# Kernel tuning notes

Measured on AMD Instinct MI355X. Metric: run time of the kernel, lower is better.

## Reference

```python
import jax, jax.numpy as jnp
import numpy as np

N_NODES = 27
SRC = jnp.array([0,1,1,1,1,2,2,2,3,3,3,4,4,4,5,5,5,5,6,6,6,6,6,7,7,7,8,8,8,9,9,9,10,10,10,11,11,11,12,12,12,13,13,13,14,14,14,15,15,15,16,16,16,17,17,17,18,18,18,18,19,20,21,21,21,22,23,23,23,24,25,26], dtype=jnp.int32)
DST = jnp.array([1,0,2,4,6,1,3,7,2,4,24,1,3,5,4,6,17,19,1,5,7,8,10,2,6,23,6,9,16,8,10,13,6,9,11,10,12,23,11,13,21,9,12,14,13,15,20,14,16,18,8,15,17,5,16,18,15,17,25,26,5,14,12,22,23,21,7,11,21,3,18,18], dtype=jnp.int32)


def _conv2d(x, w, b):
    # x: [BN, Cin, H, W], w: [Cout, Cin, 3, 3] -> SAME padding conv
    y = jax.lax.conv_general_dilated(x, w, window_strides=(1, 1), padding='SAME',
                                     dimension_numbers=('NCHW', 'OIHW', 'NCHW'))
    return y + b[None, :, None, None]


def _block(h, w, b):
    # h: [B, N, Cin, H, W]; Conv2dMessage (conv -> scatter-add over edges) + LeakyReLU(0.2) + MaxPool2d(2)
    B, N, C, H, W = h.shape
    y = _conv2d(h.reshape(B * N, C, H, W), w, b).reshape(B, N, -1, H, W)
    # propagate with aggr='add': out[dst] += y[src]; isolated-in nodes become zero
    agg = jnp.zeros_like(y).at[:, DST].add(y[:, SRC])
    a = jax.nn.leaky_relu(agg, negative_slope=0.2)
    Co = a.shape[2]
    p = jax.lax.reduce_window(a.reshape(B * N, Co, H, W), -jnp.inf, jax.lax.max,
                              (1, 1, 2, 2), (1, 1, 2, 2), 'VALID')
    return p.reshape(B, N, Co, H // 2, W // 2)


def setup_inputs() -> dict:
    key = jax.random.key(0)
    ks = jax.random.split(key, 9)
    B, Cin, H, W = 32, 4, 64, 64
    x = jax.random.normal(ks[0], (B, Cin, H, W), dtype=jnp.float32)
    def kaiming(k, shape):
        fan_in = int(np.prod(shape[1:]))
        bound = float(np.sqrt(6.0 / fan_in))
        return jax.random.uniform(k, shape, jnp.float32, -bound, bound)
    w1 = kaiming(ks[1], (32, Cin, 3, 3)); b1 = jnp.zeros((32,), jnp.float32)
    w2 = kaiming(ks[2], (64, 32, 3, 3));  b2 = jnp.zeros((64,), jnp.float32)
    w3 = kaiming(ks[3], (128, 64, 3, 3)); b3 = jnp.zeros((128,), jnp.float32)
    wc = kaiming(ks[4], (1, 128));        bc = jnp.zeros((1,), jnp.float32)
    return {"x": x, "w1": w1, "b1": b1, "w2": w2, "b2": b2,
            "w3": w3, "b3": b3, "wc": wc, "bc": bc}


def reference(x, w1, b1, w2, b2, w3, b3, wc, bc):
    B = x.shape[0]
    # torch.tile(xi, (27,1,1,1)) vectorized over batch -> [B, 27, C, H, W]
    h = jnp.broadcast_to(x[:, None], (B, N_NODES) + x.shape[1:])
    h = _block(h, w1, b1)   # [B, 27, 32, 32, 32]
    h = _block(h, w2, b2)   # [B, 27, 64, 16, 16]
    h = _block(h, w3, b3)   # [B, 27, 128, 8, 8]
    feat = h.mean(axis=(3, 4))                 # AdaptiveAvgPool2d(1) + flatten -> [B, 27, 128]
    logits = jnp.einsum('bnc,oc->bno', feat, wc) + bc  # [B, 27, 1]
    return logits[:, 0, :]                     # classifier(xi)[0] per sample -> [B, 1]
```

## Files before the change

### kernel.cpp

```cpp
#include <hip/hip_runtime.h>


#define LRELU(v) fmaxf((v), 0.2f * (v))

#define P1H_ELEMS (32 * 32 * 34 * 36)
#define P2H_ELEMS (32 * 64 * 18 * 20)

__global__ __launch_bounds__(256, 4) void k1(const float* __restrict__ x,
                                             const float* __restrict__ w1,
                                             const float* __restrict__ b1,
                                             float* __restrict__ P1H,
                                             float* __restrict__ out) {
    __shared__ __align__(16) float obuf[1152];
    const int bx = blockIdx.x;
    const int b  = blockIdx.y;
    const int rb = bx & 3, cog = bx >> 2;
    const int t  = threadIdx.x;
    const int l  = t & 63, wv = t >> 6;
    const int r  = l >> 4, q = l & 15;
    const int row0 = 16 * rb + 4 * wv + r;

    if (bx == 0 && t == 0) out[b] = 0.f;

    for (int i = t; i < 288; i += 256)
        *(float4*)&obuf[4 * i] = make_float4(0.f, 0.f, 0.f, 0.f);
    __syncthreads();

    const bool cL = (q > 0), cR = (q < 15);
    const int colL = max(4 * q - 2, 0);
    const int colR = min(4 * q + 4, 62);

    float acc[4][4];
    #pragma unroll
    for (int g = 0; g < 4; ++g) {
        float bias = b1[cog * 4 + g];
        acc[g][0] = bias; acc[g][1] = bias; acc[g][2] = bias; acc[g][3] = bias;
    }

    #pragma unroll
    for (int c = 0; c < 4; ++c) {
        float win[3][6];
        #pragma unroll
        for (int d = 0; d < 3; ++d) {
            int gr = row0 - 1 + d;
            bool v = (unsigned)gr < 64u;
            int grc = min(max(gr, 0), 63);
            const float* row = x + ((b * 4 + c) * 64 + grc) * 64;
            float2 L  = *(const float2*)(row + colL);
            float4 M  = *(const float4*)(row + 4 * q);
            float2 R2 = *(const float2*)(row + colR);
            win[d][0] = (v && cL) ? L.y : 0.f;
            win[d][1] = v ? M.x : 0.f;
            win[d][2] = v ? M.y : 0.f;
            win[d][3] = v ? M.z : 0.f;
            win[d][4] = v ? M.w : 0.f;
            win[d][5] = (v && cR) ? R2.x : 0.f;
        }
        #pragma unroll
        for (int g = 0; g < 4; ++g) {
            const float* wp = &w1[((cog * 4 + g) * 4 + c) * 9];
            #pragma unroll
            for (int d = 0; d < 3; ++d)
                #pragma unroll
                for (int j = 0; j < 3; ++j) {
                    float w = wp[3 * d + j];
                    acc[g][0] += w * win[d][j];
                    acc[g][1] += w * win[d][j + 1];
                    acc[g][2] += w * win[d][j + 2];
                    acc[g][3] += w * win[d][j + 3];
                }
        }
    }

    const int prow_l = 2 * wv + (r >> 1);
    #pragma unroll
    for (int g = 0; g < 4; ++g) {
        float m0 = fmaxf(LRELU(acc[g][0]), LRELU(acc[g][1]));
        float m1 = fmaxf(LRELU(acc[g][2]), LRELU(acc[g][3]));
        float p0 = fmaxf(m0, __shfl_xor(m0, 16));
        float p1 = fmaxf(m1, __shfl_xor(m1, 16));
        if ((r & 1) == 0) {
            obuf[(g * 8 + prow_l) * 36 + 2 * q + 1] = 12.f * p0;
            obuf[(g * 8 + prow_l) * 36 + 2 * q + 2] = 12.f * p1;
        }
    }
    __syncthreads();

    for (int i = t; i < 288; i += 256) {
        int co_l = i / 72, rem = i % 72, pr = rem / 9, cw = rem % 9;
        *(float4*)&P1H[((b * 32 + cog * 4 + co_l) * 34 + 8 * rb + pr + 1) * 36 + 4 * cw] =
            *(const float4*)&obuf[4 * i];
    }
    if (rb == 0 || rb == 3) {
        int h = rb ? 33 : 0;
        for (int i = t; i < 36; i += 256) {
            int co_l = i / 9, cw = i % 9;
            *(float4*)&P1H[((b * 32 + cog * 4 + co_l) * 34 + h) * 36 + 4 * cw] =
                make_float4(0.f, 0.f, 0.f, 0.f);
        }
    }
}

__global__ __launch_bounds__(256, 2) void k2(const float* __restrict__ P1H,
                                             const float* __restrict__ w2,
                                             const float* __restrict__ b2,
                                             float* __restrict__ p2H) {
    __shared__ __align__(16) float wtile[6144];
    __shared__ __align__(16) float xin[2880];
    __shared__ __align__(16) float obuf[1280];
    const int bx = blockIdx.x;
    const int b  = blockIdx.y;
    const int cog = bx >> 2, rs = bx & 3;
    const int c0  = cog * 16;
    const int t  = threadIdx.x, l = t & 63;
    const int wvs = __builtin_amdgcn_readfirstlane(t >> 6);
    const int q  = l & 7, R = l >> 3;

    for (int i = t; i < 1152; i += 256) {
        float4 v = *(const float4*)&w2[cog * 4608 + 4 * i];
        int e = 4 * i;
        wtile[((e + 0) / 9) * 12 + (e + 0) % 9] = v.x;
        wtile[((e + 1) / 9) * 12 + (e + 1) % 9] = v.y;
        wtile[((e + 2) / 9) * 12 + (e + 2) % 9] = v.z;
        wtile[((e + 3) / 9) * 12 + (e + 3) % 9] = v.w;
    }
    for (int i = t; i < 320; i += 256)
        *(float4*)&obuf[4 * i] = make_float4(0.f, 0.f, 0.f, 0.f);

    float acc[4][4];
    #pragma unroll
    for (int g = 0; g < 4; ++g) {
        float bias = 4.f * b2[c0 + wvs * 4 + g];
        acc[g][0] = bias; acc[g][1] = bias; acc[g][2] = bias; acc[g][3] = bias;
    }

    for (int cc = 0; cc < 4; ++cc) {
        __syncthreads();
        for (int i = t; i < 720; i += 256) {
            int cin_l = i / 90, rem = i % 90;
            *(float4*)&xin[cin_l * 360 + 4 * rem] =
                *(const float4*)&P1H[((b * 32 + cc * 8 + cin_l) * 34 + rs * 8) * 36 + 4 * rem];
        }
        __syncthreads();
        #pragma unroll
        for (int cl = 0; cl < 8; ++cl) {
            float win[3][6];
            #pragma unroll
            for (int d = 0; d < 3; ++d) {
                const float* xr = &xin[cl * 360 + (R + d) * 36 + 4 * q];
                float4 M  = *(const float4*)xr;
                float2 Rt = *(const float2*)(xr + 4);
                win[d][0] = M.x; win[d][1] = M.y; win[d][2] = M.z;
                win[d][3] = M.w; win[d][4] = Rt.x; win[d][5] = Rt.y;
            }
            const int cin = cc * 8 + cl;
            #pragma unroll
            for (int g = 0; g < 4; ++g) {
                const float* wg = &wtile[((wvs * 4 + g) * 32 + cin) * 12];
                float4 wa = *(const float4*)wg;
                float4 wb = *(const float4*)(wg + 4);
                float  w8 = wg[8];
                float wt[9] = {wa.x, wa.y, wa.z, wa.w, wb.x, wb.y, wb.z, wb.w, w8};
                #pragma unroll
                for (int d = 0; d < 3; ++d)
                    #pragma unroll
                    for (int j = 0; j < 3; ++j) {
                        float w = wt[3 * d + j];
                        acc[g][0] += w * win[d][j];
                        acc[g][1] += w * win[d][j + 1];
                        acc[g][2] += w * win[d][j + 2];
                        acc[g][3] += w * win[d][j + 3];
                    }
            }
        }
    }

    #pragma unroll
    for (int g = 0; g < 4; ++g) {
        float m0 = fmaxf(LRELU(acc[g][0]), LRELU(acc[g][1]));
        float m1 = fmaxf(LRELU(acc[g][2]), LRELU(acc[g][3]));
        float p0 = fmaxf(m0, __shfl_xor(m0, 8));
        float p1 = fmaxf(m1, __shfl_xor(m1, 8));
        if ((R & 1) == 0) {
            int co_l = wvs * 4 + g;
            obuf[(co_l * 4 + (R >> 1)) * 20 + 2 * q + 1] = p0;
            obuf[(co_l * 4 + (R >> 1)) * 20 + 2 * q + 2] = p1;
        }
    }
    __syncthreads();

    for (int i = t; i < 320; i += 256) {
        int co_l = i / 20, rem = i % 20, pr = rem / 5, cw = rem % 5;
        *(float4*)&p2H[((b * 64 + c0 + co_l) * 18 + rs * 4 + pr + 1) * 20 + 4 * cw] =
            *(const float4*)&obuf[4 * i];
    }
    if (rs == 0 || rs == 3) {
        int h2 = rs ? 17 : 0;
        for (int i = t; i < 80; i += 256) {
            int co_l = i / 5, cw = i % 5;
            *(float4*)&p2H[((b * 64 + c0 + co_l) * 18 + h2) * 20 + 4 * cw] =
                make_float4(0.f, 0.f, 0.f, 0.f);
        }
    }
}

__global__ __launch_bounds__(256, 4) void k3(const float* __restrict__ p2H,
                                             const float* __restrict__ w3,
                                             const float* __restrict__ b3,
                                             const float* __restrict__ wc,
                                             const float* __restrict__ bc,
                                             float* __restrict__ out) {
    __shared__ __align__(16) float smem[3072];
    const int cog = blockIdx.x;
    const int b   = blockIdx.y;
    const int c0  = cog * 4;
    const int t   = threadIdx.x, l = t & 63;
    const int wvs = __builtin_amdgcn_readfirstlane(t >> 6);
    const int r   = l >> 2, q = l & 3;

    for (int i = t; i < 576; i += 256) {
        float4 v = *(const float4*)&w3[cog * 2304 + 4 * i];
        int e = 4 * i;
        smem[((e + 0) / 9) * 12 + (e + 0) % 9] = v.x;
        smem[((e + 1) / 9) * 12 + (e + 1) % 9] = v.y;
        smem[((e + 2) / 9) * 12 + (e + 2) % 9] = v.z;
        smem[((e + 3) / 9) * 12 + (e + 3) % 9] = v.w;
    }
    __syncthreads();

    float acc[4][4];
    #pragma unroll
    for (int g = 0; g < 4; ++g) {
        float bias = (wvs == 0) ? b3[c0 + g] : 0.f;
        acc[g][0] = bias; acc[g][1] = bias; acc[g][2] = bias; acc[g][3] = bias;
    }

    #pragma unroll
    for (int cl = 0; cl < 16; ++cl) {
        const int cin = wvs * 16 + cl;
        const float* pb = p2H + (((b * 64 + cin) * 18 + r) * 20 + 4 * q);
        float win[3][6];
        #pragma unroll
        for (int d = 0; d < 3; ++d) {
            float4 M  = *(const float4*)(pb + d * 20);
            float2 Rt = *(const float2*)(pb + d * 20 + 4);
            win[d][0] = M.x; win[d][1] = M.y; win[d][2] = M.z;
            win[d][3] = M.w; win[d][4] = Rt.x; win[d][5] = Rt.y;
        }
        #pragma unroll
        for (int g = 0; g < 4; ++g) {
            const float* wg = &smem[(g * 64 + cin) * 12];
            float4 wa = *(const float4*)wg;
            float4 wb = *(const float4*)(wg + 4);
            float  w8 = wg[8];
            float wt[9] = {wa.x, wa.y, wa.z, wa.w, wb.x, wb.y, wb.z, wb.w, w8};
            #pragma unroll
            for (int d = 0; d < 3; ++d)
                #pragma unroll
                for (int j = 0; j < 3; ++j) {
                    float w = wt[3 * d + j];
                    acc[g][0] += w * win[d][j];
                    acc[g][1] += w * win[d][j + 1];
                    acc[g][2] += w * win[d][j + 2];
                    acc[g][3] += w * win[d][j + 3];
                }
        }
    }

    __syncthreads();
    if (wvs > 0) {
        float* cb = &smem[((wvs - 1) * 64 + l) * 16];
        #pragma unroll
        for (int g = 0; g < 4; ++g)
            *(float4*)&cb[g * 4] =
                make_float4(acc[g][0], acc[g][1], acc[g][2], acc[g][3]);
    }
    __syncthreads();

    if (wvs == 0) {
        #pragma unroll
        for (int k = 0; k < 3; ++k) {
            const float* cb = &smem[(k * 64 + l) * 16];
            #pragma unroll
            for (int g = 0; g < 4; ++g) {
                float4 v = *(const float4*)&cb[g * 4];
                acc[g][0] += v.x; acc[g][1] += v.y;
                acc[g][2] += v.z; acc[g][3] += v.w;
            }
        }
        float vsum = 0.f;
        #pragma unroll
        for (int g = 0; g < 4; ++g) {
            float m0 = fmaxf(LRELU(acc[g][0]), LRELU(acc[g][1]));
            float m1 = fmaxf(LRELU(acc[g][2]), LRELU(acc[g][3]));
            float pm0 = fmaxf(m0, __shfl_xor(m0, 4));
            float pm1 = fmaxf(m1, __shfl_xor(m1, 4));
            float contrib = ((r & 1) == 0) ? (pm0 + pm1) : 0.f;
            vsum += contrib * wc[c0 + g];
        }
        #pragma unroll
        for (int off = 32; off > 0; off >>= 1) vsum += __shfl_xor(vsum, off);
        if (l == 0) {
            float o = vsum * (1.f / 64.f);
            if (cog == 0) o += bc[0];
            atomicAdd(&out[b], o);
        }
    }
}

extern "C" void kernel_launch(void* const* d_in, const int* in_sizes, int n_in,
                              void* d_out, int out_size, void* d_ws, size_t ws_size,
                              hipStream_t stream) {
    const float* x  = (const float*)d_in[0];
    const float* w1 = (const float*)d_in[1];
    const float* b1 = (const float*)d_in[2];
    const float* w2 = (const float*)d_in[3];
    const float* b2 = (const float*)d_in[4];
    const float* w3 = (const float*)d_in[5];
    const float* b3 = (const float*)d_in[6];
    const float* wc = (const float*)d_in[7];
    const float* bc = (const float*)d_in[8];
    float* out = (float*)d_out;

    float* P1H = (float*)d_ws;
    float* p2H = P1H + P1H_ELEMS;

    k1<<<dim3(32, 32), 256, 0, stream>>>(x, w1, b1, P1H, out);
    k2<<<dim3(16, 32), 256, 0, stream>>>(P1H, w2, b2, p2H);
    k3<<<dim3(32, 32), 256, 0, stream>>>(p2H, w3, b3, wc, bc, out);
}
```

Measured before the change: 138.6 us.

## Split k2 input channels across waves with scalar weight loads and cross-wave reduction

k2 now gives each block 8 row-slabs instead of 4 and loads all 32 input channels of its 6-row slab into shared memory once. Each wave handles 8 input channels for all 16 output channels, reading weights as wave-uniform scalar loads from global memory, and the four partial sums are reduced through shared memory. k3 likewise drops its shared-memory weight staging in favour of uniform global weight loads and uses a padded reduction buffer. The goal is to double the number of k2 blocks, cut shared-memory use and remove the weight-staging pass, in exchange for a cross-wave reduction step and more scalar-load traffic.

Measured after the change: 131.2 us. 5.3% less time.

```diff
diff --git a/kernel.cpp b/kernel.cpp
--- a/kernel.cpp
+++ b/kernel.cpp
@@ -16,8 +16,8 @@
     const int b  = blockIdx.y;
     const int rb = bx & 3, cog = bx >> 2;
     const int t  = threadIdx.x;
-    const int l  = t & 63, wv = t >> 6;
-    const int r  = l >> 4, q = l & 15;
+    const int l = t & 63, wv = t >> 6;
+    const int r = l >> 4, q = l & 15;
     const int row0 = 16 * rb + 4 * wv + r;
 
     if (bx == 0 && t == 0) out[b] = 0.f;
@@ -101,104 +101,105 @@
     }
 }
 
-__global__ __launch_bounds__(256, 2) void k2(const float* __restrict__ P1H,
+__global__ __launch_bounds__(256, 4) void k2(const float* __restrict__ P1H,
                                              const float* __restrict__ w2,
                                              const float* __restrict__ b2,
                                              float* __restrict__ p2H) {
-    __shared__ __align__(16) float wtile[6144];
-    __shared__ __align__(16) float xin[2880];
-    __shared__ __align__(16) float obuf[1280];
+    __shared__ __align__(16) float xin[6912];
+    __shared__ __align__(16) float obuf[640];
     const int bx = blockIdx.x;
     const int b  = blockIdx.y;
-    const int cog = bx >> 2, rs = bx & 3;
+    const int cog = bx >> 3, rs = bx & 7;
     const int c0  = cog * 16;
-    const int t  = threadIdx.x, l = t & 63;
+    const int t = threadIdx.x, l = t & 63;
     const int wvs = __builtin_amdgcn_readfirstlane(t >> 6);
-    const int q  = l & 7, R = l >> 3;
-
-    for (int i = t; i < 1152; i += 256) {
-        float4 v = *(const float4*)&w2[cog * 4608 + 4 * i];
-        int e = 4 * i;
-        wtile[((e + 0) / 9) * 12 + (e + 0) % 9] = v.x;
-        wtile[((e + 1) / 9) * 12 + (e + 1) % 9] = v.y;
-        wtile[((e + 2) / 9) * 12 + (e + 2) % 9] = v.z;
-        wtile[((e + 3) / 9) * 12 + (e + 3) % 9] = v.w;
-    }
-    for (int i = t; i < 320; i += 256)
+    const int ql = l & 15, R = l >> 4;
+
+    for (int i = t; i < 1728; i += 256) {
+        int cin = i / 54, rem = i % 54, r = rem / 9, cw = rem % 9;
+        *(float4*)&xin[cin * 216 + r * 36 + 4 * cw] =
+            *(const float4*)&P1H[((b * 32 + cin) * 34 + rs * 4 + r) * 36 + 4 * cw];
+    }
+    for (int i = t; i < 160; i += 256)
         *(float4*)&obuf[4 * i] = make_float4(0.f, 0.f, 0.f, 0.f);
-
-    float acc[4][4];
-    #pragma unroll
-    for (int g = 0; g < 4; ++g) {
-        float bias = 4.f * b2[c0 + wvs * 4 + g];
-        acc[g][0] = bias; acc[g][1] = bias; acc[g][2] = bias; acc[g][3] = bias;
-    }
-
-    for (int cc = 0; cc < 4; ++cc) {
-        __syncthreads();
-        for (int i = t; i < 720; i += 256) {
-            int cin_l = i / 90, rem = i % 90;
-            *(float4*)&xin[cin_l * 360 + 4 * rem] =
-                *(const float4*)&P1H[((b * 32 + cc * 8 + cin_l) * 34 + rs * 8) * 36 + 4 * rem];
-        }
-        __syncthreads();
-        #pragma unroll
-        for (int cl = 0; cl < 8; ++cl) {
-            float win[3][6];
-            #pragma unroll
-            for (int d = 0; d < 3; ++d) {
-                const float* xr = &xin[cl * 360 + (R + d) * 36 + 4 * q];
-                float4 M  = *(const float4*)xr;
-                float2 Rt = *(const float2*)(xr + 4);
-                win[d][0] = M.x; win[d][1] = M.y; win[d][2] = M.z;
-                win[d][3] = M.w; win[d][4] = Rt.x; win[d][5] = Rt.y;
+    __syncthreads();
+
+    float acc[16][2];
+    #pragma unroll
+    for (int co = 0; co < 16; ++co) {
+        float bias = (wvs == 0) ? 4.f * b2[c0 + co] : 0.f;
+        acc[co][0] = bias; acc[co][1] = bias;
+    }
+
+    #pragma unroll 2
+    for (int cl = 0; cl < 8; ++cl) {
+        const int cin = wvs * 8 + cl;
+        float win[3][4];
+        #pragma unroll
+        for (int d = 0; d < 3; ++d) {
+            const float* xr = &xin[cin * 216 + (R + d) * 36 + 2 * ql];
+            float2 a0 = *(const float2*)xr;
+            float2 a1 = *(const float2*)(xr + 2);
+            win[d][0] = a0.x; win[d][1] = a0.y; win[d][2] = a1.x; win[d][3] = a1.y;
+        }
+        const int wbase = __builtin_amdgcn_readfirstlane((c0 * 32 + cin) * 9);
+        #pragma unroll
+        for (int co = 0; co < 16; ++co) {
+            const float* wg = w2 + wbase + co * 288;
+            float wt[9];
+            #pragma unroll
+            for (int k = 0; k < 9; ++k) wt[k] = wg[k];
+            #pragma unroll
+            for (int d = 0; d < 3; ++d)
+                #pragma unroll
+                for (int j = 0; j < 3; ++j) {
+                    float w = wt[3 * d + j];
+                    acc[co][0] += w * win[d][j];
+                    acc[co][1] += w * win[d][j + 1];
+                }
+        }
+    }
+
+    __syncthreads();
+    if (wvs > 0) {
+        float* cb = &xin[((wvs - 1) * 64 + l) * 36];
+        #pragma unroll
+        for (int g = 0; g < 8; ++g)
+            *(float4*)&cb[4 * g] = make_float4(acc[2 * g][0], acc[2 * g][1],
+                                               acc[2 * g + 1][0], acc[2 * g + 1][1]);
+    }
+    __syncthreads();
+    if (wvs == 0) {
+        #pragma unroll
+        for (int k = 0; k < 3; ++k) {
+            const float* cb = &xin[(k * 64 + l) * 36];
+            #pragma unroll
+            for (int g = 0; g < 8; ++g) {
+                float4 v = *(const float4*)&cb[4 * g];
+                acc[2 * g][0] += v.x; acc[2 * g][1] += v.y;
+                acc[2 * g + 1][0] += v.z; acc[2 * g + 1][1] += v.w;
             }
-            const int cin = cc * 8 + cl;
-            #pragma unroll
-            for (int g = 0; g < 4; ++g) {
-                const float* wg = &wtile[((wvs * 4 + g) * 32 + cin) * 12];
-                float4 wa = *(const float4*)wg;
-                float4 wb = *(const float4*)(wg + 4);
-                float  w8 = wg[8];
-                float wt[9] = {wa.x, wa.y, wa.z, wa.w, wb.x, wb.y, wb.z, wb.w, w8};
-                #pragma unroll
-                for (int d = 0; d < 3; ++d)
-                    #pragma unroll
-                    for (int j = 0; j < 3; ++j) {
-                        float w = wt[3 * d + j];
-                        acc[g][0] += w * win[d][j];
-                        acc[g][1] += w * win[d][j + 1];
-                        acc[g][2] += w * win[d][j + 2];
-                        acc[g][3] += w * win[d][j + 3];
-                    }
-            }
-        }
-    }
-
-    #pragma unroll
-    for (int g = 0; g < 4; ++g) {
-        float m0 = fmaxf(LRELU(acc[g][0]), LRELU(acc[g][1]));
-        float m1 = fmaxf(LRELU(acc[g][2]), LRELU(acc[g][3]));
-        float p0 = fmaxf(m0, __shfl_xor(m0, 8));
-        float p1 = fmaxf(m1, __shfl_xor(m1, 8));
-        if ((R & 1) == 0) {
-            int co_l = wvs * 4 + g;
-            obuf[(co_l * 4 + (R >> 1)) * 20 + 2 * q + 1] = p0;
-            obuf[(co_l * 4 + (R >> 1)) * 20 + 2 * q + 2] = p1;
-        }
-    }
-    __syncthreads();
-
-    for (int i = t; i < 320; i += 256) {
-        int co_l = i / 20, rem = i % 20, pr = rem / 5, cw = rem % 5;
-        *(float4*)&p2H[((b * 64 + c0 + co_l) * 18 + rs * 4 + pr + 1) * 20 + 4 * cw] =
+        }
+        #pragma unroll
+        for (int co = 0; co < 16; ++co) {
+            float m = fmaxf(LRELU(acc[co][0]), LRELU(acc[co][1]));
+            float p = fmaxf(m, __shfl_xor(m, 16));
+            if ((R & 1) == 0)
+                obuf[(co * 2 + (R >> 1)) * 20 + ql + 1] = p;
+        }
+    }
+    __syncthreads();
+
+    for (int i = t; i < 160; i += 256) {
+        int co = i / 10, rem = i % 10, pr = rem / 5, cw = rem % 5;
+        *(float4*)&p2H[((b * 64 + c0 + co) * 18 + rs * 2 + 1 + pr) * 20 + 4 * cw] =
             *(const float4*)&obuf[4 * i];
     }
-    if (rs == 0 || rs == 3) {
+    if (rs == 0 || rs == 7) {
         int h2 = rs ? 17 : 0;
         for (int i = t; i < 80; i += 256) {
-            int co_l = i / 5, cw = i % 5;
-            *(float4*)&p2H[((b * 64 + c0 + co_l) * 18 + h2) * 20 + 4 * cw] =
+            int co = i / 5, cw = i % 5;
+            *(float4*)&p2H[((b * 64 + c0 + co) * 18 + h2) * 20 + 4 * cw] =
                 make_float4(0.f, 0.f, 0.f, 0.f);
         }
     }
@@ -210,7 +211,7 @@
                                              const float* __restrict__ wc,
                                              const float* __restrict__ bc,
                                              float* __restrict__ out) {
-    __shared__ __align__(16) float smem[3072];
+    __shared__ __align__(16) float cbuf[3840];
     const int cog = blockIdx.x;
     const int b   = blockIdx.y;
     const int c0  = cog * 4;
@@ -218,16 +219,6 @@
     const int wvs = __builtin_amdgcn_readfirstlane(t >> 6);
     const int r   = l >> 2, q = l & 3;
 
-    for (int i = t; i < 576; i += 256) {
-        float4 v = *(const float4*)&w3[cog * 2304 + 4 * i];
-        int e = 4 * i;
-        smem[((e + 0) / 9) * 12 + (e + 0) % 9] = v.x;
-        smem[((e + 1) / 9) * 12 + (e + 1) % 9] = v.y;
-        smem[((e + 2) / 9) * 12 + (e + 2) % 9] = v.z;
-        smem[((e + 3) / 9) * 12 + (e + 3) % 9] = v.w;
-    }
-    __syncthreads();
-
     float acc[4][4];
     #pragma unroll
     for (int g = 0; g < 4; ++g) {
@@ -235,7 +226,7 @@
         acc[g][0] = bias; acc[g][1] = bias; acc[g][2] = bias; acc[g][3] = bias;
     }
 
-    #pragma unroll
+    #pragma unroll 4
     for (int cl = 0; cl < 16; ++cl) {
         const int cin = wvs * 16 + cl;
         const float* pb = p2H + (((b * 64 + cin) * 18 + r) * 20 + 4 * q);
@@ -247,13 +238,13 @@
             win[d][0] = M.x; win[d][1] = M.y; win[d][2] = M.z;
             win[d][3] = M.w; win[d][4] = Rt.x; win[d][5] = Rt.y;
         }
+        const int wbase = __builtin_amdgcn_readfirstlane((c0 * 64 + cin) * 9);
         #pragma unroll
         for (int g = 0; g < 4; ++g) {
-            const float* wg = &smem[(g * 64 + cin) * 12];
-            float4 wa = *(const float4*)wg;
-            float4 wb = *(const float4*)(wg + 4);
-            float  w8 = wg[8];
-            float wt[9] = {wa.x, wa.y, wa.z, wa.w, wb.x, wb.y, wb.z, wb.w, w8};
+            const float* wg = w3 + wbase + g * 576;
+            float wt[9];
+            #pragma unroll
+            for (int k = 0; k < 9; ++k) wt[k] = wg[k];
             #pragma unroll
             for (int d = 0; d < 3; ++d)
                 #pragma unroll
@@ -267,12 +258,11 @@
         }
     }
 
-    __syncthreads();
     if (wvs > 0) {
-        float* cb = &smem[((wvs - 1) * 64 + l) * 16];
+        float* cb = &cbuf[((wvs - 1) * 64 + l) * 20];
         #pragma unroll
         for (int g = 0; g < 4; ++g)
-            *(float4*)&cb[g * 4] =
+            *(float4*)&cb[4 * g] =
                 make_float4(acc[g][0], acc[g][1], acc[g][2], acc[g][3]);
     }
     __syncthreads();
@@ -280,10 +270,10 @@
     if (wvs == 0) {
         #pragma unroll
         for (int k = 0; k < 3; ++k) {
-            const float* cb = &smem[(k * 64 + l) * 16];
+            const float* cb = &cbuf[(k * 64 + l) * 20];
             #pragma unroll
             for (int g = 0; g < 4; ++g) {
-                float4 v = *(const float4*)&cb[g * 4];
+                float4 v = *(const float4*)&cb[4 * g];
                 acc[g][0] += v.x; acc[g][1] += v.y;
                 acc[g][2] += v.z; acc[g][3] += v.w;
             }
@@ -326,6 +316,6 @@
     float* p2H = P1H + P1H_ELEMS;
 
     k1<<<dim3(32, 32), 256, 0, stream>>>(x, w1, b1, P1H, out);
-    k2<<<dim3(16, 32), 256, 0, stream>>>(P1H, w2, b2, p2H);
+    k2<<<dim3(32, 32), 256, 0, stream>>>(P1H, w2, b2, p2H);
     k3<<<dim3(32, 32), 256, 0, stream>>>(p2H, w3, b3, wc, bc, out);
 }
```
